# Kernel optimization log

Hardware: AMD Instinct MI355X
Metric: run time of the kernel (lower is better)

The kernel has to match this reference:

```python
import jax, jax.numpy as jnp
import numpy as np

GAMMA = 2.0
ALPHA = 0.25
NEG_TH = 0.4
POS_TH = 0.5
NUM_CLASSES = 80
STRIDES = [8, 16, 32, 64, 128]
IMG_H, IMG_W = 800, 1024
LEVEL_HW = [(100, 128), (50, 64), (25, 32), (13, 16), (7, 8)]


def _base_anchors(stride):
    # standard RetinaNet: octave_base_scale=4, 3 scales/octave, ratios 0.5/1/2
    scales = 4.0 * stride * np.array([2 ** 0, 2 ** (1.0 / 3), 2 ** (2.0 / 3)])
    ratios = np.array([0.5, 1.0, 2.0])
    h_r = np.sqrt(ratios)
    w_r = 1.0 / h_r
    ws = (w_r[:, None] * scales[None, :]).reshape(-1)
    hs = (h_r[:, None] * scales[None, :]).reshape(-1)
    return np.stack([-ws / 2, -hs / 2, ws / 2, hs / 2], axis=1)  # [9,4]


def build_anchors():
    out = []
    for (h, w), s in zip(LEVEL_HW, STRIDES):
        base = _base_anchors(s)
        xs = (np.arange(w) + 0.5) * s
        ys = (np.arange(h) + 0.5) * s
        cx, cy = np.meshgrid(xs, ys)  # [h,w]
        ctr = np.stack([cx, cy, cx, cy], axis=-1)  # [h,w,4]
        a = ctr[:, :, None, :] + base[None, None, :, :]  # [h,w,9,4] anchor-fastest
        out.append(a.reshape(-1, 4))
    return jnp.asarray(np.concatenate(out, axis=0), dtype=jnp.float32)  # [A,4]


def _iou(gt, an):  # [G,4],[A,4] -> [G,A]
    lt = jnp.maximum(gt[:, None, :2], an[None, :, :2])
    rb = jnp.minimum(gt[:, None, 2:], an[None, :, 2:])
    wh = jnp.clip(rb - lt, 0.0)
    inter = wh[..., 0] * wh[..., 1]
    area_g = (gt[:, 2] - gt[:, 0]) * (gt[:, 3] - gt[:, 1])
    area_a = (an[:, 2] - an[:, 0]) * (an[:, 3] - an[:, 1])
    return inter / (area_g[:, None] + area_a[None, :] - inter + 1e-6)


def _encode(an, gt):  # delta encoding, mean=0 std=1
    aw = an[:, 2] - an[:, 0]
    ah = an[:, 3] - an[:, 1]
    ax = (an[:, 0] + an[:, 2]) * 0.5
    ay = (an[:, 1] + an[:, 3]) * 0.5
    gw = gt[:, 2] - gt[:, 0]
    gh = gt[:, 3] - gt[:, 1]
    gx = (gt[:, 0] + gt[:, 2]) * 0.5
    gy = (gt[:, 1] + gt[:, 3]) * 0.5
    return jnp.stack([(gx - ax) / aw, (gy - ay) / ah, jnp.log(gw / aw), jnp.log(gh / ah)], axis=1)


def _per_image(logits, regp, gtb, gtl, anchors):
    G = gtb.shape[0]
    iou = _iou(gtb, anchors)  # [G,A]
    max_ov = iou.max(axis=0)
    arg_ov = iou.argmax(axis=0)
    assigned = jnp.where(max_ov < NEG_TH, 0, -1)
    assigned = jnp.where(max_ov >= POS_TH, arg_ov + 1, assigned)
    max_gt = iou.max(axis=1)
    eq = iou == max_gt[:, None]
    any_eq = eq.any(axis=0)
    last_j = (G - 1) - jnp.argmax(eq[::-1], axis=0)
    assigned = jnp.where(any_eq, last_j + 1, assigned)
    pos = assigned > 0
    neg = assigned == 0
    gi = jnp.clip(assigned - 1, 0, G - 1)
    labels = jnp.where(pos, gtl[gi], NUM_CLASSES)  # negatives get label = num_classes
    include = (pos | neg).astype(logits.dtype)  # ignored anchors contribute 0
    # focal loss
    p = jnp.clip(jax.nn.sigmoid(logits), 1e-6, 1.0 - 1e-6)
    cr = jnp.arange(NUM_CLASSES)[None, :]
    t = labels[:, None]
    term1 = (1.0 - p) ** GAMMA * jnp.log(p)
    term2 = p ** GAMMA * jnp.log(1.0 - p)
    per = -(t == cr).astype(p.dtype) * term1 * ALPHA - ((t != cr) & (t >= 0)).astype(p.dtype) * term2 * (1.0 - ALPHA)
    cls_sum = (per.sum(axis=1) * include).sum()
    # smooth-free L1 on positives
    reg_t = _encode(anchors, gtb[gi])
    reg_sum = (jnp.abs(regp - reg_t).sum(axis=1) * pos.astype(regp.dtype)).sum()
    return cls_sum, reg_sum, pos.sum()


def _flatten_levels(levels, c):
    n = levels[0].shape[0]
    return jnp.concatenate([p.transpose(0, 2, 3, 1).reshape(n, -1, c) for p in levels], axis=1)


def reference(cls_p0, cls_p1, cls_p2, cls_p3, cls_p4, reg_p0, reg_p1, reg_p2, reg_p3, reg_p4, gt_bboxes, gt_labels):
    anchors = build_anchors()
    cls = _flatten_levels([cls_p0, cls_p1, cls_p2, cls_p3, cls_p4], NUM_CLASSES)  # [N,A,80]
    reg = _flatten_levels([reg_p0, reg_p1, reg_p2, reg_p3, reg_p4], 4)  # [N,A,4]
    cls_s, reg_s, npos = jax.vmap(lambda l, r, b, t: _per_image(l, r, b, t, anchors))(cls, reg, gt_bboxes, gt_labels)
    num_pos = jnp.maximum(npos.sum(), 1).astype(cls.dtype)
    return (cls_s.sum() / num_pos, reg_s.sum() / num_pos)


def setup_inputs() -> dict:
    key = jax.random.key(0)
    ks = jax.random.split(key, 16)
    N, G = 2, 32
    d = {}
    for i, (h, w) in enumerate(LEVEL_HW):
        d[f"cls_p{i}"] = jax.random.normal(ks[i], (N, 9 * NUM_CLASSES, h, w), jnp.float32)
        d[f"reg_p{i}"] = jax.random.normal(ks[5 + i], (N, 9 * 4, h, w), jnp.float32)
    cx = jax.random.uniform(ks[10], (N, G), minval=50.0, maxval=IMG_W - 50.0)
    cy = jax.random.uniform(ks[11], (N, G), minval=50.0, maxval=IMG_H - 50.0)
    bw = jax.random.uniform(ks[12], (N, G), minval=32.0, maxval=300.0)
    bh = jax.random.uniform(ks[13], (N, G), minval=32.0, maxval=300.0)
    x1 = jnp.clip(cx - bw / 2, 0.0, IMG_W - 2.0)
    y1 = jnp.clip(cy - bh / 2, 0.0, IMG_H - 2.0)
    x2 = jnp.clip(cx + bw / 2, x1 + 1.0, float(IMG_W))
    y2 = jnp.clip(cy + bh / 2, y1 + 1.0, float(IMG_H))
    d["gt_bboxes"] = jnp.stack([x1, y1, x2, y2], axis=-1)
    d["gt_labels"] = jax.random.randint(ks[14], (N, G), 0, NUM_CLASSES)
    return d
```

## Files before the change

kernel.cpp:

```cpp
#include <hip/hip_runtime.h>
#include <stdint.h>

namespace {
constexpr int A_TOTAL = 153576;
constexpr int NG      = 32;
constexpr int NIMG    = 2;
constexpr int NCLS    = 80;

constexpr size_t WS_CLS0  = 0;
constexpr size_t WS_REG   = 2048;
constexpr size_t WS_NPOS  = 2056;
constexpr size_t WS_MAXGT = 2112;
constexpr size_t WS_LABEL = 2560;
constexpr size_t WS_ZERO  = 2560;
}

__device__ __attribute__((noinline)) float4 anchor_box(int idx) {
    int base, W, stride;
    if      (idx < 115200) { base = 0;      W = 128; stride = 8;   }
    else if (idx < 144000) { base = 115200; W = 64;  stride = 16;  }
    else if (idx < 151200) { base = 144000; W = 32;  stride = 32;  }
    else if (idx < 153072) { base = 151200; W = 16;  stride = 64;  }
    else                   { base = 153072; W = 8;   stride = 128; }
    int s    = idx - base;
    int cell = s / 9;
    int a    = s - cell * 9;
    int y    = cell / W;
    int x    = cell - y * W;
    int r    = a / 3;
    int k    = a - r * 3;
    double c3 = (k == 0) ? 1.0 : ((k == 1) ? 1.2599210498948731648 : 1.5874010519681994748);
    double hr = (r == 0) ? 0.70710678118654752440 : ((r == 1) ? 1.0 : 1.4142135623730950488);
    double scale = 4.0 * (double)stride * c3;
    double wr  = 1.0 / hr;
    double wsz = wr * scale;
    double hsz = hr * scale;
    double cx  = ((double)x + 0.5) * (double)stride;
    double cy  = ((double)y + 0.5) * (double)stride;
    float4 out;
    out.x = (float)(cx - wsz / 2.0);
    out.y = (float)(cy - hsz / 2.0);
    out.z = (float)(cx + wsz / 2.0);
    out.w = (float)(cy + hsz / 2.0);
    return out;
}

__device__ __attribute__((noinline)) float iou_fn(float4 an, float4 g) {
    float ltx = fmaxf(g.x, an.x), lty = fmaxf(g.y, an.y);
    float rbx = fminf(g.z, an.z), rby = fminf(g.w, an.w);
    float w = fmaxf(rbx - ltx, 0.f), h = fmaxf(rby - lty, 0.f);
    float inter = w * h;
    float ag = (g.z - g.x) * (g.w - g.y);
    float aa = (an.z - an.x) * (an.w - an.y);
    return inter / (ag + aa - inter + 1e-6f);
}

__global__ __launch_bounds__(256)
void kmaxgt(const float* __restrict__ gtb, unsigned* __restrict__ maxgt) {
    int n   = blockIdx.y;
    int tid = threadIdx.x;
    int anchor = blockIdx.x * 256 + tid;
    __shared__ float4   g_s[NG];
    __shared__ unsigned smax[NG];
    if (tid < NG) {
        g_s[tid]  = ((const float4*)gtb)[n * NG + tid];
        smax[tid] = 0u;
    }
    __syncthreads();
    bool  valid = anchor < A_TOTAL;
    float4 an = anchor_box(valid ? anchor : 0);
    int lane = tid & 63;
    for (int j = 0; j < NG; ++j) {
        float iou = valid ? iou_fn(an, g_s[j]) : 0.f;
        for (int off = 32; off; off >>= 1)
            iou = fmaxf(iou, __shfl_xor(iou, off));
        if (lane == 0) atomicMax(&smax[j], __float_as_uint(iou));
    }
    __syncthreads();
    if (tid < NG) atomicMax(&maxgt[n * NG + tid], smax[tid]);
}

__global__ __launch_bounds__(256)
void kassign(const float* __restrict__ gtb, const int* __restrict__ gtl,
             const float* __restrict__ maxgt, uint8_t* __restrict__ labels,
             const float* __restrict__ r0, const float* __restrict__ r1,
             const float* __restrict__ r2, const float* __restrict__ r3,
             const float* __restrict__ r4,
             double* __restrict__ reg_acc, int* __restrict__ npos_acc) {
    int n   = blockIdx.y;
    int tid = threadIdx.x;
    int anchor = blockIdx.x * 256 + tid;
    __shared__ float4 g_s[NG];
    __shared__ float  mg_s[NG];
    __shared__ int    gl_s[NG];
    if (tid < NG) {
        g_s[tid]  = ((const float4*)gtb)[n * NG + tid];
        mg_s[tid] = maxgt[n * NG + tid];
        gl_s[tid] = gtl[n * NG + tid];
    }
    __syncthreads();
    bool  valid = anchor < A_TOTAL;
    float4 an = anchor_box(valid ? anchor : 0);
    float best = -1.f; int arg = 0; int last = -1;
    for (int j = 0; j < NG; ++j) {
        float iou = iou_fn(an, g_s[j]);
        if (iou > best) { best = iou; arg = j; }
        if (iou == mg_s[j]) last = j;
    }
    int assigned = -1;
    if (best < 0.4f)  assigned = 0;
    if (best >= 0.5f) assigned = arg + 1;
    if (last >= 0)    assigned = last + 1;

    float rsum = 0.f; bool pos = false;
    if (valid) {
        int base, HW; const float* rp;
        if      (anchor < 115200) { base = 0;      HW = 12800; rp = r0; }
        else if (anchor < 144000) { base = 115200; HW = 3200;  rp = r1; }
        else if (anchor < 151200) { base = 144000; HW = 800;   rp = r2; }
        else if (anchor < 153072) { base = 151200; HW = 208;   rp = r3; }
        else                      { base = 153072; HW = 56;    rp = r4; }
        int s = anchor - base;
        int cell = s / 9; int a = s - cell * 9;

        uint8_t lab;
        if (assigned > 0) {
            pos = true;
            int gi = assigned - 1;
            lab = (uint8_t)gl_s[gi];
            float aw = an.z - an.x, ah = an.w - an.y;
            float ax = (an.x + an.z) * 0.5f, ay = (an.y + an.w) * 0.5f;
            float4 g = g_s[gi];
            float gw = g.z - g.x, gh = g.w - g.y;
            float gx = (g.x + g.z) * 0.5f, gy = (g.y + g.w) * 0.5f;
            float t0 = (gx - ax) / aw, t1 = (gy - ay) / ah;
            float t2 = __logf(gw / aw), t3 = __logf(gh / ah);
            long off = (long)(n * 36 + a * 4) * HW + cell;
            float p0 = rp[off], p1 = rp[off + HW], p2 = rp[off + 2 * HW], p3 = rp[off + 3 * HW];
            rsum = fabsf(p0 - t0) + fabsf(p1 - t1) + fabsf(p2 - t2) + fabsf(p3 - t3);
        } else {
            lab = (assigned == 0) ? (uint8_t)NCLS : (uint8_t)255;
        }
        labels[n * A_TOTAL + base + a * HW + cell] = lab;
    }
    for (int off = 32; off; off >>= 1) rsum += __shfl_xor(rsum, off);
    unsigned long long bal = __ballot(pos);
    __shared__ float pr[4];
    __shared__ int   pn[4];
    int wid = tid >> 6;
    if ((tid & 63) == 0) { pr[wid] = rsum; pn[wid] = __popcll(bal); }
    __syncthreads();
    if (tid == 0) {
        float s = pr[0] + pr[1] + pr[2] + pr[3];
        int   c = pn[0] + pn[1] + pn[2] + pn[3];
        atomicAdd(reg_acc, (double)s);
        atomicAdd(npos_acc, c);
    }
}

__device__ __forceinline__ float focal(float z, int c, int lab) {
    float e   = __expf(z);
    float u   = 1.f + e;
    float inv = __builtin_amdgcn_rcpf(u);
    float L   = __logf(u);
    float p   = e * inv;
    float t2  = 0.75f * (p * p) * L;
    float t1  = 0.25f * (inv * inv) * (L - z);
    float r   = (c == lab) ? t1 : t2;
    return (lab == 255) ? 0.f : r;
}

template <int HW, int BASE, int BPL>
__device__ float cls_level(const float* __restrict__ cp,
                           const uint8_t* __restrict__ labels, int rel) {
    int slab  = rel / BPL;
    int chunk = rel - slab * BPL;
    int n = slab / 9, a = slab - 9 * n;
    int cell = chunk * 128 + 2 * (int)threadIdx.x;
    if (cell >= HW) return 0.f;
    int lb = n * A_TOTAL + BASE + a * HW + cell;
    int lab0 = labels[lb], lab1 = labels[lb + 1];
    const float* p = cp + (size_t)(n * 720 + a * 80) * HW + cell;
    float acc = 0.f;
#pragma unroll 8
    for (int c = 0; c < NCLS; ++c, p += HW) {
        float2 z = *(const float2*)p;
        acc += focal(z.x, c, lab0);
        acc += focal(z.y, c, lab1);
    }
    return acc;
}

__global__ __launch_bounds__(64)
void kcls(const float* __restrict__ c0, const float* __restrict__ c1,
          const float* __restrict__ c2, const float* __restrict__ c3,
          const float* __restrict__ c4,
          const uint8_t* __restrict__ labels, char* __restrict__ ws) {
    int b = blockIdx.x;
    float v;
    if      (b < 1800) v = cls_level<12800, 0,      100>(c0, labels, b);
    else if (b < 2250) v = cls_level<3200,  115200, 25 >(c1, labels, b - 1800);
    else if (b < 2376) v = cls_level<800,   144000, 7  >(c2, labels, b - 2250);
    else if (b < 2412) v = cls_level<208,   151200, 2  >(c3, labels, b - 2376);
    else               v = cls_level<56,    153072, 1  >(c4, labels, b - 2412);
    for (int off = 32; off; off >>= 1) v += __shfl_xor(v, off);
    if (threadIdx.x == 0)
        atomicAdd((double*)(ws + WS_CLS0 + (size_t)(b & 7) * 256), (double)v);
}

__global__ void kfinal(const char* __restrict__ ws, float* __restrict__ out) {
    double cls = 0.0;
    for (int i = 0; i < 8; ++i) cls += *(const double*)(ws + WS_CLS0 + (size_t)i * 256);
    double reg = *(const double*)(ws + WS_REG);
    int    np  = *(const int*)(ws + WS_NPOS);
    float denom = (float)(np > 1 ? np : 1);
    out[0] = (float)cls / denom;
    out[1] = (float)reg / denom;
}

extern "C" void kernel_launch(void* const* d_in, const int* in_sizes, int n_in,
                              void* d_out, int out_size, void* d_ws, size_t ws_size,
                              hipStream_t stream) {
    static const int HWs[5] = {12800, 3200, 800, 208, 56};
    const float* cls_p[5] = {nullptr, nullptr, nullptr, nullptr, nullptr};
    const float* reg_p[5] = {nullptr, nullptr, nullptr, nullptr, nullptr};
    const float* gtb = nullptr;
    const int*   gtl = nullptr;
    for (int i = 0; i < n_in; ++i) {
        int sz = in_sizes[i];
        if (sz == NIMG * NG * 4) { gtb = (const float*)d_in[i]; continue; }
        if (sz == NIMG * NG)     { gtl = (const int*)d_in[i];   continue; }
        for (int l = 0; l < 5; ++l) {
            if (sz == NIMG * 9 * NCLS * HWs[l]) { cls_p[l] = (const float*)d_in[i]; break; }
            if (sz == NIMG * 9 * 4 * HWs[l])    { reg_p[l] = (const float*)d_in[i]; break; }
        }
    }
    float* out = (float*)d_out;

    char* ws = (char*)d_ws;
    hipMemsetAsync(d_ws, 0, WS_ZERO, stream);
    unsigned* maxgt_u = (unsigned*)(ws + WS_MAXGT);
    float*    maxgt_f = (float*)(ws + WS_MAXGT);
    uint8_t*  labels  = (uint8_t*)(ws + WS_LABEL);
    double*   reg_acc = (double*)(ws + WS_REG);
    int*      npos    = (int*)(ws + WS_NPOS);

    dim3 gAB((A_TOTAL + 255) / 256, NIMG);
    kmaxgt<<<gAB, 256, 0, stream>>>(gtb, maxgt_u);
    kassign<<<gAB, 256, 0, stream>>>(gtb, gtl, maxgt_f, labels,
                                     reg_p[0], reg_p[1], reg_p[2], reg_p[3], reg_p[4],
                                     reg_acc, npos);
    kcls<<<2430, 64, 0, stream>>>(cls_p[0], cls_p[1], cls_p[2], cls_p[3], cls_p[4],
                                  labels, ws);
    kfinal<<<1, 1, 0, stream>>>(ws, out);
}
```

Measured before the change: 217.5 us.

## Widen cls loads to float4, fuse final reduction via last-block counter

Each thread in the classification loss kernel now handles four anchors with float4 loads and a uchar4 label load, which halves the block count. The separate final kernel is removed: each block bumps an atomic counter after adding its partial sum, and the last block reads the accumulators and writes the output. Anchor-box division by grid width is also replaced with shifts. This removes one kernel launch and makes the memory accesses wider, at the cost of fewer blocks in flight and a dependency on the counter being zeroed by the memset.

```diff
diff --git a/kernel.cpp b/kernel.cpp
--- a/kernel.cpp
+++ b/kernel.cpp
@@ -6,27 +6,29 @@
 constexpr int NG      = 32;
 constexpr int NIMG    = 2;
 constexpr int NCLS    = 80;
+constexpr int NBLK_CLS = 1242;
 
 constexpr size_t WS_CLS0  = 0;
 constexpr size_t WS_REG   = 2048;
 constexpr size_t WS_NPOS  = 2056;
+constexpr size_t WS_CNT   = 2060;
 constexpr size_t WS_MAXGT = 2112;
 constexpr size_t WS_LABEL = 2560;
 constexpr size_t WS_ZERO  = 2560;
 }
 
 __device__ __attribute__((noinline)) float4 anchor_box(int idx) {
-    int base, W, stride;
-    if      (idx < 115200) { base = 0;      W = 128; stride = 8;   }
-    else if (idx < 144000) { base = 115200; W = 64;  stride = 16;  }
-    else if (idx < 151200) { base = 144000; W = 32;  stride = 32;  }
-    else if (idx < 153072) { base = 151200; W = 16;  stride = 64;  }
-    else                   { base = 153072; W = 8;   stride = 128; }
+    int base, lw, stride;
+    if      (idx < 115200) { base = 0;      lw = 7; stride = 8;   }
+    else if (idx < 144000) { base = 115200; lw = 6; stride = 16;  }
+    else if (idx < 151200) { base = 144000; lw = 5; stride = 32;  }
+    else if (idx < 153072) { base = 151200; lw = 4; stride = 64;  }
+    else                   { base = 153072; lw = 3; stride = 128; }
     int s    = idx - base;
     int cell = s / 9;
     int a    = s - cell * 9;
-    int y    = cell / W;
-    int x    = cell - y * W;
+    int y    = cell >> lw;
+    int x    = cell - (y << lw);
     int r    = a / 3;
     int k    = a - r * 3;
     double c3 = (k == 0) ? 1.0 : ((k == 1) ? 1.2599210498948731648 : 1.5874010519681994748);
@@ -176,17 +178,19 @@
     int slab  = rel / BPL;
     int chunk = rel - slab * BPL;
     int n = slab / 9, a = slab - 9 * n;
-    int cell = chunk * 128 + 2 * (int)threadIdx.x;
+    int cell = chunk * 256 + 4 * (int)threadIdx.x;
     if (cell >= HW) return 0.f;
     int lb = n * A_TOTAL + BASE + a * HW + cell;
-    int lab0 = labels[lb], lab1 = labels[lb + 1];
+    uchar4 lab4 = *(const uchar4*)(labels + lb);
     const float* p = cp + (size_t)(n * 720 + a * 80) * HW + cell;
     float acc = 0.f;
 #pragma unroll 8
     for (int c = 0; c < NCLS; ++c, p += HW) {
-        float2 z = *(const float2*)p;
-        acc += focal(z.x, c, lab0);
-        acc += focal(z.y, c, lab1);
+        float4 z = *(const float4*)p;
+        acc += focal(z.x, c, lab4.x);
+        acc += focal(z.y, c, lab4.y);
+        acc += focal(z.z, c, lab4.z);
+        acc += focal(z.w, c, lab4.w);
     }
     return acc;
 }
@@ -195,27 +199,31 @@
 void kcls(const float* __restrict__ c0, const float* __restrict__ c1,
           const float* __restrict__ c2, const float* __restrict__ c3,
           const float* __restrict__ c4,
-          const uint8_t* __restrict__ labels, char* __restrict__ ws) {
+          const uint8_t* __restrict__ labels, char* __restrict__ ws,
+          float* __restrict__ out) {
     int b = blockIdx.x;
     float v;
-    if      (b < 1800) v = cls_level<12800, 0,      100>(c0, labels, b);
-    else if (b < 2250) v = cls_level<3200,  115200, 25 >(c1, labels, b - 1800);
-    else if (b < 2376) v = cls_level<800,   144000, 7  >(c2, labels, b - 2250);
-    else if (b < 2412) v = cls_level<208,   151200, 2  >(c3, labels, b - 2376);
-    else               v = cls_level<56,    153072, 1  >(c4, labels, b - 2412);
+    if      (b < 900)  v = cls_level<12800, 0,      50>(c0, labels, b);
+    else if (b < 1134) v = cls_level<3200,  115200, 13>(c1, labels, b - 900);
+    else if (b < 1206) v = cls_level<800,   144000, 4 >(c2, labels, b - 1134);
+    else if (b < 1224) v = cls_level<208,   151200, 1 >(c3, labels, b - 1206);
+    else               v = cls_level<56,    153072, 1 >(c4, labels, b - 1224);
     for (int off = 32; off; off >>= 1) v += __shfl_xor(v, off);
-    if (threadIdx.x == 0)
+    if (threadIdx.x == 0) {
         atomicAdd((double*)(ws + WS_CLS0 + (size_t)(b & 7) * 256), (double)v);
-}
-
-__global__ void kfinal(const char* __restrict__ ws, float* __restrict__ out) {
-    double cls = 0.0;
-    for (int i = 0; i < 8; ++i) cls += *(const double*)(ws + WS_CLS0 + (size_t)i * 256);
-    double reg = *(const double*)(ws + WS_REG);
-    int    np  = *(const int*)(ws + WS_NPOS);
-    float denom = (float)(np > 1 ? np : 1);
-    out[0] = (float)cls / denom;
-    out[1] = (float)reg / denom;
+        __threadfence();
+        unsigned done = atomicAdd((unsigned*)(ws + WS_CNT), 1u);
+        if (done == NBLK_CLS - 1) {
+            double cls = 0.0;
+            for (int i = 0; i < 8; ++i)
+                cls += atomicAdd((double*)(ws + WS_CLS0 + (size_t)i * 256), 0.0);
+            double reg = atomicAdd((double*)(ws + WS_REG), 0.0);
+            int    np  = atomicAdd((int*)(ws + WS_NPOS), 0);
+            float denom = (float)(np > 1 ? np : 1);
+            out[0] = (float)cls / denom;
+            out[1] = (float)reg / denom;
+        }
+    }
 }
 
 extern "C" void kernel_launch(void* const* d_in, const int* in_sizes, int n_in,
@@ -250,7 +258,6 @@
     kassign<<<gAB, 256, 0, stream>>>(gtb, gtl, maxgt_f, labels,
                                      reg_p[0], reg_p[1], reg_p[2], reg_p[3], reg_p[4],
                                      reg_acc, npos);
-    kcls<<<2430, 64, 0, stream>>>(cls_p[0], cls_p[1], cls_p[2], cls_p[3], cls_p[4],
-                                  labels, ws);
-    kfinal<<<1, 1, 0, stream>>>(ws, out);
-}
+    kcls<<<NBLK_CLS, 64, 0, stream>>>(cls_p[0], cls_p[1], cls_p[2], cls_p[3], cls_p[4],
+                                      labels, ws, out);
+}
```

Measured after the change: 289.3 us. 33.0% more time.
